# Optimization experiments

Measured on AMD Instinct MI355X. Metric: run time of the kernel, lower is better.

The kernel has to match this reference:

```python
import jax, jax.numpy as jnp
import numpy as np

B, S, D, C, I = 2, 1024, 1024, 64, 2048
N = S // C            # num_chunks (S divisible by C -> no padding)
EPS = 1e-6
BASE_LR = 0.01


def setup_inputs() -> dict:
    key = jax.random.key(0)
    ks = jax.random.split(key, 12)
    def xavier(k, shape):
        fan_in = shape[-1]
        return jax.random.normal(k, shape, jnp.float32) * (1.0 / np.sqrt(fan_in))
    return {
        "x": jax.random.normal(ks[0], (B, S, D), jnp.float32),
        "w1": xavier(ks[1], (I, D)),          # memory layer 0 weight [out,in]
        "w2": xavier(ks[2], (D, I)),          # memory layer 1 weight
        "ln_w": jnp.ones((D,), jnp.float32),  # memory RMSNorm weight
        "wq": xavier(ks[3], (D, D)),
        "wk": xavier(ks[4], (D, D)),
        "wv": xavier(ks[5], (D, D)),
        "qn_w": jnp.ones((D,), jnp.float32),
        "kn_w": jnp.ones((D,), jnp.float32),
        "alpha_w": jax.random.normal(ks[6], (1, C * D), jnp.float32) * 1e-3,
        "theta_w": jax.random.normal(ks[7], (1, C * D), jnp.float32) * 1e-3,
        "eta_w": jax.random.normal(ks[8], (1, C * D), jnp.float32) * 1e-3,
    }


def _rms(x, w):
    return x * jax.lax.rsqrt(jnp.mean(x * x, axis=-1, keepdims=True) + EPS) * w


def _memory_fwd(params, x):
    # 2-layer MLP memory with RMSNorm + residual
    w1, w2, lnw = params
    h = jax.nn.silu(x @ w1.T)
    y = h @ w2.T
    return x + _rms(y, lnw)


def _comb(e1, e2):
    # binary_operator: (a_j*a_i, kv_j + a_j*kv_i)
    a_i, kv_i = e1
    a_j, kv_j = e2
    return (a_j * a_i, kv_j + a_j * kv_i)


def _assocscan_update(pm, ps, g, eta, alpha):
    # pm,ps: [B,*s], g: [B,N,*s], eta/alpha: [B,N]
    extra = g.ndim - 2
    e = eta.reshape(eta.shape + (1,) * extra)
    a = alpha.reshape(alpha.shape + (1,) * extra)
    ones = jnp.ones_like(e[:, :1])
    # surprise recurrence: S_t = eta_t * S_{t-1} - g_t
    cS = jnp.concatenate([ones, e], axis=1)
    vS = jnp.concatenate([ps[:, None], -g], axis=1)
    _, Ssec = jax.lax.associative_scan(_comb, (cS, vS), axis=1)
    # memory recurrence: M_t = (1-alpha_t) * M_{t-1} + S_t
    cM = jnp.concatenate([ones, 1.0 - a], axis=1)
    vM = jnp.concatenate([pm[:, None], Ssec[:, 1:]], axis=1)
    _, Msec = jax.lax.associative_scan(_comb, (cM, vM), axis=1)
    return Msec[:, -1], Ssec[:, -1]


def reference(x, w1, w2, ln_w, wq, wk, wv, qn_w, kn_w, alpha_w, theta_w, eta_w):
    x4 = x.reshape(B, N, C, D)
    xc = x4.reshape(B, N, C * D)
    alpha = jax.nn.sigmoid(xc @ alpha_w.T)[..., 0]           # [B,N]
    theta = jax.nn.sigmoid(xc @ theta_w.T) * BASE_LR         # [B,N,1]
    eta = jax.nn.sigmoid(xc @ eta_w.T)[..., 0]               # [B,N]

    k = _rms(jax.nn.silu(x4 @ wk.T), kn_w)                   # [B,N,C,D]
    v = jax.nn.silu(x4 @ wv.T)                               # [B,N,C,D]

    # batched memory params (get_memory_params expands over batch)
    bw1 = jnp.broadcast_to(w1, (B,) + w1.shape)
    bw2 = jnp.broadcast_to(w2, (B,) + w2.shape)
    bln = jnp.broadcast_to(ln_w, (B,) + ln_w.shape)
    # initial surprises = 0
    s1 = jnp.zeros_like(bw1)
    s2 = jnp.zeros_like(bw2)
    sl = jnp.zeros_like(bln)

    def loss(p, ki, vi, th):
        pred = _memory_fwd(p, ki)
        return jnp.sum(jnp.mean((vi - pred) ** 2 * th, axis=-1))

    per_sample_grad = jax.vmap(jax.vmap(jax.grad(loss), in_axes=(None, 0, 0, 0)),
                               in_axes=(0, 0, 0, 0))
    g1, g2, gl = per_sample_grad((bw1, bw2, bln), k, v, theta)  # [B,N,*param]

    nw1, ns1 = _assocscan_update(bw1, s1, g1, eta, alpha)
    nw2, ns2 = _assocscan_update(bw2, s2, g2, eta, alpha)
    nln, nsl = _assocscan_update(bln, sl, gl, eta, alpha)

    # retrieve with updated memory
    q = _rms(jax.nn.silu(x4 @ wq.T), qn_w)                   # [B,N,C,D]
    out = jax.vmap(_memory_fwd)((nw1, nw2, nln), q)          # [B,N,C,D]
    out = out.reshape(B, S, D)
    return (out, nw1, nw2, nln, ns1, ns2, nsl)
```

## Files before the change

### kernel.cpp

```cpp
#include <hip/hip_runtime.h>

#define KD 1024
#define KI 2048
#define KB 2
#define KS 1024
#define KC 64
#define KN 16
#define KEPS 1e-6f

typedef __bf16 bf16x8 __attribute__((ext_vector_type(8)));
typedef __bf16 bf16x4 __attribute__((ext_vector_type(4)));
typedef float f32x4 __attribute__((ext_vector_type(4)));

__device__ __forceinline__ float sigf(float x){ return 1.0f/(1.0f+__expf(-x)); }
__device__ __forceinline__ float siluf(float x){ return x*sigf(x); }
__device__ __forceinline__ float dsiluf(float x){ float s=sigf(x); return s*(1.0f+x*(1.0f-s)); }

__device__ __forceinline__ void gld16(const __bf16* g, __bf16* l) {
  __builtin_amdgcn_global_load_lds(
    (const __attribute__((address_space(1))) unsigned int*)g,
    (__attribute__((address_space(3))) unsigned int*)l, 16, 0, 0);
}

#define WAIT_VM8()  asm volatile("s_waitcnt vmcnt(8)" ::: "memory")
#define WAIT_VM6()  asm volatile("s_waitcnt vmcnt(6)" ::: "memory")
#define WAIT_VM0()  asm volatile("s_waitcnt vmcnt(0)" ::: "memory")
#define WAIT_LGKM() asm volatile("s_waitcnt lgkmcnt(0)" ::: "memory")
#define BAR()       __builtin_amdgcn_s_barrier()

__device__ __forceinline__ void tconv_bodyP(float* T, const __bf16* in, __bf16* out,
                                            int R, int Cc, int bx, int by)
{
  const int r0 = by*64, c0 = bx*64;
  const int tx = threadIdx.x & 15, ty = threadIdx.x >> 4;
  #pragma unroll
  for (int i=0;i<4;i++){
    const int r = r0 + ty + i*16;
    const bf16x4 v = *(const bf16x4*)(in + (size_t)r*Cc + c0 + tx*4);
    T[(ty+i*16)*65 + tx*4+0]=(float)v[0]; T[(ty+i*16)*65 + tx*4+1]=(float)v[1];
    T[(ty+i*16)*65 + tx*4+2]=(float)v[2]; T[(ty+i*16)*65 + tx*4+3]=(float)v[3];
  }
  __syncthreads();
  #pragma unroll
  for (int i=0;i<4;i++){
    bf16x4 o = { (__bf16)T[(tx*4+0)*65 + ty+i*16], (__bf16)T[(tx*4+1)*65 + ty+i*16],
                 (__bf16)T[(tx*4+2)*65 + ty+i*16], (__bf16)T[(tx*4+3)*65 + ty+i*16] };
    *(bf16x4*)(out + (size_t)(c0+ty+i*16)*R + r0 + tx*4) = o;
  }
}

__device__ __forceinline__ void tconv_bodyF(const float* in, __bf16* out,
                                            int R, int Cc, int bx, int by)
{
  __shared__ float T[64][65];
  const int r0 = by*64, c0 = bx*64;
  const int tx = threadIdx.x & 15, ty = threadIdx.x >> 4;
  #pragma unroll
  for (int i=0;i<4;i++){
    const int r = r0 + ty + i*16;
    const float4 v = *(const float4*)(in + (size_t)r*Cc + c0 + tx*4);
    T[ty+i*16][tx*4+0]=v.x; T[ty+i*16][tx*4+1]=v.y;
    T[ty+i*16][tx*4+2]=v.z; T[ty+i*16][tx*4+3]=v.w;
  }
  __syncthreads();
  #pragma unroll
  for (int i=0;i<4;i++){
    bf16x4 o = { (__bf16)T[tx*4+0][ty+i*16], (__bf16)T[tx*4+1][ty+i*16],
                 (__bf16)T[tx*4+2][ty+i*16], (__bf16)T[tx*4+3][ty+i*16] };
    *(bf16x4*)(out + (size_t)(c0+ty+i*16)*R + r0 + tx*4) = o;
  }
}

__global__ __launch_bounds__(256) void prep_kernel(
  const float* __restrict__ x, const float* __restrict__ wk, const float* __restrict__ wv,
  const float* __restrict__ wq, const float* __restrict__ w1, const float* __restrict__ w2,
  const float* __restrict__ aw, const float* __restrict__ tw, const float* __restrict__ ew,
  __bf16* __restrict__ xb, __bf16* __restrict__ wkb, __bf16* __restrict__ wvb,
  __bf16* __restrict__ wqb, __bf16* __restrict__ w1b, __bf16* __restrict__ w2b,
  __bf16* __restrict__ w2tb, float* __restrict__ part, float* __restrict__ gl)
{
  const int g = blockIdx.x;
  if (g < 2048) {
    const int i = g*256 + threadIdx.x;
    const float4 xv = *(const float4*)(x + (size_t)i*4);
    bf16x4 o = { (__bf16)xv.x, (__bf16)xv.y, (__bf16)xv.z, (__bf16)xv.w };
    *(bf16x4*)(xb + (size_t)i*4) = o;
    const size_t co = (size_t)(i & 16383) * 4;
    const float4 av = *(const float4*)(aw + co);
    const float4 tv = *(const float4*)(tw + co);
    const float4 ev = *(const float4*)(ew + co);
    float da = xv.x*av.x + xv.y*av.y + xv.z*av.z + xv.w*av.w;
    float dt = xv.x*tv.x + xv.y*tv.y + xv.z*tv.z + xv.w*tv.w;
    float de = xv.x*ev.x + xv.y*ev.y + xv.z*ev.z + xv.w*ev.w;
    __shared__ float sA[256], sT[256], sE[256];
    sA[threadIdx.x]=da; sT[threadIdx.x]=dt; sE[threadIdx.x]=de;
    __syncthreads();
    for (int s=128;s>0;s>>=1){
      if ((int)threadIdx.x < s){
        sA[threadIdx.x]+=sA[threadIdx.x+s];
        sT[threadIdx.x]+=sT[threadIdx.x+s];
        sE[threadIdx.x]+=sE[threadIdx.x+s];
      }
      __syncthreads();
    }
    if (threadIdx.x==0){
      part[g] = sA[0]; part[2048+g] = sT[0]; part[4096+g] = sE[0];
    }
  } else if (g < 9216) {
    const long t = (long)g*256 + threadIdx.x;
    const float* s; __bf16* d; long i;
    if (t < 786432)       { s=wk; d=wkb; i=t-524288; }
    else if (t < 1048576) { s=wv; d=wvb; i=t-786432; }
    else if (t < 1310720) { s=wq; d=wqb; i=t-1048576; }
    else if (t < 1835008) { s=w1; d=w1b; i=t-1310720; }
    else                  { s=w2; d=w2b; i=t-1835008; }
    const float4 v = *(const float4*)(s + i*4);
    bf16x4 o = { (__bf16)v.x, (__bf16)v.y, (__bf16)v.z, (__bf16)v.w };
    *(bf16x4*)(d + i*4) = o;
  } else if (g < 9728) {
    const int gg = g - 9216;
    tconv_bodyF(w2, w2tb, 1024, 2048, gg & 31, gg >> 5);
  } else {
    const int gg = g - 9728;
    float4 z = {0.f,0.f,0.f,0.f};
    *(float4*)(gl + (size_t)gg*1024 + threadIdx.x*4) = z;
  }
}

template<int EPI, int MODE, int WT>
__device__ __forceinline__ void mgemm_body(
    __bf16* As, __bf16* Bs,
    const __bf16* __restrict__ A, const __bf16* __restrict__ B0,
    const __bf16* __restrict__ B1, const __bf16* __restrict__ B2,
    float* __restrict__ F0, float* __restrict__ F1,
    __bf16* __restrict__ Oa, __bf16* __restrict__ Ob, const __bf16* __restrict__ Aux,
    __bf16* __restrict__ OT, int ldt,
    int M, int Nn, int lda, int ldb, long bstr,
    int bx, int by, int bz)
{
  const int n0 = bx * 128;
  const int m0 = by * 128;
  const __bf16* Bp = B0;
  if (MODE==1) { if (bz==1) Bp=B1; else if (bz==2) Bp=B2; }
  float* F0p = F0;
  int koff0 = 0;
  if (MODE==2) koff0 = bz << 10;
  Bp += (size_t)(m0 >> 10) * (size_t)bstr;
  const int tid = threadIdx.x, wv = tid >> 6, lane = tid & 63;
  const int wm = (wv >> 1) << 6, wn = (wv & 1) << 6;
  const int fr = lane & 15, fg = lane >> 4;
  const int lr = lane >> 3, lc = lane & 7;
  const __bf16* asrc[4]; __bf16* adst[4];
  const __bf16* bsrc[4]; __bf16* bdst[4];
  #pragma unroll
  for (int i=0;i<4;i++){
    const int rowbase=(wv*4+i)*8, row=rowbase+lr;
    asrc[i] = A + (size_t)(m0+row)*lda + koff0 + ((lc^(row&7))<<3);
    adst[i] = As + rowbase*64;
    bsrc[i] = Bp + (size_t)(n0+row)*ldb + koff0 + ((lc^(row&7))<<3);
    bdst[i] = Bs + rowbase*64;
  }
  f32x4 acc[4][4] = {};
  #pragma unroll
  for (int i=0;i<4;i++) gld16(asrc[i], adst[i]);
  #pragma unroll
  for (int i=0;i<4;i++) gld16(bsrc[i], bdst[i]);
  WAIT_VM0();
  BAR();
  #pragma unroll 2
  for (int t=0;t<16;++t){
    const int p = t & 1;
    if (t < 15){
      const int ko = (t+1) << 6;
      const int q = p ^ 1;
      #pragma unroll
      for (int i=0;i<4;i++) gld16(asrc[i]+ko, adst[i]+q*8192);
      #pragma unroll
      for (int i=0;i<4;i++) gld16(bsrc[i]+ko, bdst[i]+q*8192);
      WAIT_VM8();
    } else {
      WAIT_VM0();
    }
    BAR();
    #pragma unroll
    for (int ks=0;ks<2;++ks){
      bf16x8 af[4], bfv[4];
      #pragma unroll
      for (int mi=0;mi<4;++mi){
        const int r = wm + mi*16 + fr;
        af[mi] = *(const bf16x8*)(As + p*8192 + r*64 + ((((ks<<2)+fg)^(r&7))<<3));
      }
      #pragma unroll
      for (int ni=0;ni<4;++ni){
        const int r = wn + ni*16 + fr;
        bfv[ni] = *(const bf16x8*)(Bs + p*8192 + r*64 + ((((ks<<2)+fg)^(r&7))<<3));
      }
      #pragma unroll
      for (int mi=0;mi<4;++mi)
        #pragma unroll
        for (int ni=0;ni<4;++ni)
          acc[mi][ni] = __builtin_amdgcn_mfma_f32_16x16x32_bf16(af[mi], bfv[ni], acc[mi][ni], 0,0,0);
    }
    WAIT_LGKM();
    BAR();
  }
  __bf16* T = As;
  #pragma unroll
  for (int mi=0;mi<4;++mi){
    #pragma unroll
    for (int ni=0;ni<4;++ni){
      bf16x4 tv;
      #pragma unroll
      for (int j=0;j<4;++j){
        const int m = m0 + wm + mi*16 + fg*4 + j;
        const int n = n0 + wn + ni*16 + fr;
        const size_t idx = (size_t)m * Nn + n;
        const float v = acc[mi][ni][j];
        float tval = 0.f;
        if (EPI==0) F0p[idx] = v;
        else if (EPI==2) { const float sv = siluf(v); Oa[idx]=(__bf16)sv; Ob[idx]=(__bf16)dsiluf(v); tval=sv; }
        else if (EPI==3) tval = v * (float)Aux[idx];
        else if (EPI==4) Oa[idx] = (__bf16)siluf(v);
        else if (EPI==5) {
          if (bz==0) F0[idx] = siluf(v);
          else if (bz==1) Oa[idx] = (__bf16)siluf(v);
          else F1[idx] = siluf(v);
        }
        else if (EPI==6) Oa[(size_t)bz*M*Nn + idx] = (__bf16)v;
        if (WT) tv[j] = (__bf16)tval;
      }
      if (WT){
        const int nl = wn + ni*16 + fr;
        const int ml = wm + mi*16 + fg*4;
        *(bf16x4*)(T + nl*128 + (ml ^ ((nl&7)<<3))) = tv;
      }
    }
  }
  if (WT){
    __syncthreads();
    const int tn = tid >> 1, tc = tid & 1;
    #pragma unroll
    for (int u=0;u<8;++u){
      const int m8 = (tc*8+u)*8;
      const bf16x8 v = *(const bf16x8*)(T + tn*128 + (m8 ^ ((tn&7)<<3)));
      *(bf16x8*)(OT + (size_t)(n0+tn)*ldt + m0 + m8) = v;
    }
  }
}

template<int EPI, int MODE, int WT>
__global__ __launch_bounds__(256) void mgemm3(
    const __bf16* __restrict__ A, const __bf16* __restrict__ B0,
    const __bf16* __restrict__ B1, const __bf16* __restrict__ B2,
    float* __restrict__ F0, float* __restrict__ F1,
    __bf16* __restrict__ Oa, __bf16* __restrict__ Ob, const __bf16* __restrict__ Aux,
    __bf16* __restrict__ OT, int ldt,
    int M, int Nn, int lda, int ldb, long bstr)
{
  __shared__ __bf16 As[2*128*64];
  __shared__ __bf16 Bs[2*128*64];
  mgemm_body<EPI,MODE,WT>(As, Bs, A, B0, B1, B2, F0, F1, Oa, Ob, Aux, OT, ldt,
                          M, Nn, lda, ldb, bstr, blockIdx.x, blockIdx.y, blockIdx.z);
}

__global__ __launch_bounds__(256) void gemm_a_kernel(
    const __bf16* __restrict__ kb16, const __bf16* __restrict__ w1b,
    __bf16* __restrict__ hb16, __bf16* __restrict__ db16, __bf16* __restrict__ hT,
    __bf16* __restrict__ kT)
{
  __shared__ __bf16 As[2*128*64];
  __shared__ __bf16 Bs[2*128*64];
  const int g = blockIdx.x;
  if (g < 256)
    mgemm_body<2,0,1>(As, Bs, kb16, w1b, nullptr, nullptr, nullptr, nullptr,
                      hb16, db16, nullptr, hT, 2048, 2048, 2048, 1024, 1024, 0,
                      g & 15, g >> 4, 0);
  else {
    const int t = g - 256;
    tconv_bodyP((float*)As, kb16, kT, 2048, 1024, t & 15, t >> 4);
  }
}

__global__ __launch_bounds__(256) void gemm_ga_kernel(
    const __bf16* __restrict__ gyb, const __bf16* __restrict__ w2tb,
    const __bf16* __restrict__ db16, __bf16* __restrict__ gaT,
    __bf16* __restrict__ gyT)
{
  __shared__ __bf16 As[2*128*64];
  __shared__ __bf16 Bs[2*128*64];
  const int g = blockIdx.x;
  if (g < 256)
    mgemm_body<3,0,1>(As, Bs, gyb, w2tb, nullptr, nullptr, nullptr, nullptr,
                      nullptr, nullptr, db16, gaT, 2048, 2048, 2048, 1024, 1024, 0,
                      g & 15, g >> 4, 0);
  else {
    const int t = g - 256;
    tconv_bodyP((float*)As, gyb, gyT, 2048, 1024, t & 15, t >> 4);
  }
}

__device__ __forceinline__ void wacc_body(
    __bf16* As, __bf16* Bs,
    const __bf16* __restrict__ A, const __bf16* __restrict__ B,
    const float* __restrict__ Winit,
    const float* __restrict__ cm, const float* __restrict__ cs,
    const float* __restrict__ Pw,
    float* __restrict__ outM, __bf16* __restrict__ outMb, float* __restrict__ outS,
    int M, int Nn, int lda, int ldb, int n0, int m0, int bz)
{
  const int koff0 = bz << 10;
  const int tid = threadIdx.x, wv = tid >> 6, lane = tid & 63;
  const int wm = (wv >> 1) << 6, wn = (wv & 1) << 5;
  const int fr = lane & 15, fg = lane >> 4;
  const int lr = lane >> 3, lc = lane & 7;
  float cmr[KN], csr[KN];
  #pragma unroll
  for (int n=0;n<KN;n++){ cmr[n]=cm[bz*KN+n]; csr[n]=cs[bz*KN+n]; }
  const __bf16* asrc[4]; __bf16* adst[4];
  const __bf16* bsrc[2]; __bf16* bdst[2];
  #pragma unroll
  for (int i=0;i<4;i++){
    const int rowbase=(wv*4+i)*8, row=rowbase+lr;
    asrc[i] = A + (size_t)(m0+row)*lda + koff0 + ((lc^(row&7))<<3);
    adst[i] = As + rowbase*64;
  }
  #pragma unroll
  for (int i=0;i<2;i++){
    const int rowbase=(wv*2+i)*8, row=rowbase+lr;
    bsrc[i] = B + (size_t)(n0+row)*ldb + koff0 + ((lc^(row&7))<<3);
    bdst[i] = Bs + rowbase*64;
  }
  f32x4 accM[4][2] = {}, accS[4][2] = {};
  asm volatile("s_waitcnt vmcnt(0) lgkmcnt(0)" ::: "memory");
  #pragma unroll
  for (int i=0;i<4;i++) gld16(asrc[i], adst[i]);
  #pragma unroll
  for (int i=0;i<2;i++) gld16(bsrc[i], bdst[i]);
  WAIT_VM0();
  BAR();
  #pragma unroll 2
  for (int t=0;t<16;++t){
    const int p = t & 1;
    const float cmc = cmr[t], csc = csr[t];
    if (t < 15){
      const int ko = (t+1) << 6;
      const int q = p ^ 1;
      #pragma unroll
      for (int i=0;i<4;i++) gld16(asrc[i]+ko, adst[i]+q*8192);
      #pragma unroll
      for (int i=0;i<2;i++) gld16(bsrc[i]+ko, bdst[i]+q*4096);
      WAIT_VM6();
    } else {
      WAIT_VM0();
    }
    BAR();
    bf16x8 a0[4], a1[4], b0[2], b1[2];
    #pragma unroll
    for (int mi=0;mi<4;++mi){
      const int r = wm + mi*16 + fr;
      a0[mi] = *(const bf16x8*)(As + p*8192 + r*64 + (((0+fg)^(r&7))<<3));
      a1[mi] = *(const bf16x8*)(As + p*8192 + r*64 + (((4+fg)^(r&7))<<3));
    }
    #pragma unroll
    for (int ni=0;ni<2;++ni){
      const int r = wn + ni*16 + fr;
      b0[ni] = *(const bf16x8*)(Bs + p*4096 + r*64 + (((0+fg)^(r&7))<<3));
      b1[ni] = *(const bf16x8*)(Bs + p*4096 + r*64 + (((4+fg)^(r&7))<<3));
    }
    #pragma unroll
    for (int mi=0;mi<4;++mi){
      #pragma unroll
      for (int ni=0;ni<2;++ni){
        const f32x4 zf = {0.f,0.f,0.f,0.f};
        f32x4 P = __builtin_amdgcn_mfma_f32_16x16x32_bf16(a0[mi], b0[ni], zf, 0,0,0);
        P = __builtin_amdgcn_mfma_f32_16x16x32_bf16(a1[mi], b1[ni], P, 0,0,0);
        accM[mi][ni] += P * cmc;
        accS[mi][ni] += P * csc;
      }
    }
    WAIT_LGKM();
    BAR();
  }
  const float pw = Pw[bz];
  #pragma unroll
  for (int mi=0;mi<4;++mi){
    #pragma unroll
    for (int ni=0;ni<2;++ni){
      #pragma unroll
      for (int j=0;j<4;++j){
        const int m = m0 + wm + mi*16 + fg*4 + j;
        const int n = n0 + wn + ni*16 + fr;
        const size_t widx = (size_t)m * Nn + n;
        const size_t oidx = (size_t)bz * M * Nn + widx;
        const float vm = pw * Winit[widx] + accM[mi][ni][j];
        outM[oidx] = vm;
        outMb[oidx] = (__bf16)vm;
        outS[oidx] = accS[mi][ni][j];
      }
    }
  }
}

__global__ __launch_bounds__(256) void waccall_kernel(
    const __bf16* __restrict__ gaT, const __bf16* __restrict__ kT, const float* __restrict__ w1,
    const __bf16* __restrict__ gyT, const __bf16* __restrict__ hT, const float* __restrict__ w2,
    const float* __restrict__ gl, const float* __restrict__ lnw,
    const float* __restrict__ cm, const float* __restrict__ cs, const float* __restrict__ Pw,
    float* __restrict__ nw1, __bf16* __restrict__ nw1b, float* __restrict__ ns1,
    float* __restrict__ nw2, __bf16* __restrict__ nw2b, float* __restrict__ ns2,
    float* __restrict__ nln, float* __restrict__ nsl)
{
  __shared__ __bf16 As[2*128*64];
  __shared__ __bf16 Bs[2*64*64];
  const int g = blockIdx.x;
  if (g < 512){
    const int bz = g >> 8, rem = g & 255;
    wacc_body(As, Bs, gaT, kT, w1, cm, cs, Pw, nw1, nw1b, ns1,
              2048, 1024, 2048, 2048, (rem & 15)*64, (rem >> 4)*128, bz);
  } else if (g < 1024){
    const int t = g - 512;
    const int bz = t >> 8, rem = t & 255;
    wacc_body(As, Bs, gyT, hT, w2, cm, cs, Pw, nw2, nw2b, ns2,
              1024, 2048, 2048, 2048, (rem & 31)*64, (rem >> 5)*128, bz);
  } else {
    const int idx = (g - 1024)*256 + threadIdx.x;
    const int b = idx >> 10, d = idx & (KD-1);
    float am=0.f, as=0.f;
    for (int n=0;n<KN;n++){
      const float gv = gl[(size_t)(b*KN+n)*KD + d];
      am += cm[b*KN+n]*gv; as += cs[b*KN+n]*gv;
    }
    nln[idx] = Pw[b]*lnw[d] + am;
    nsl[idx] = as;
  }
}

__global__ __launch_bounds__(256) void rmsfuse_kernel(
    const float* __restrict__ kv, const float* __restrict__ kw, __bf16* __restrict__ k16,
    const float* __restrict__ qv, const float* __restrict__ qw, __bf16* __restrict__ q16,
    const float* __restrict__ part, float* __restrict__ cm, float* __restrict__ cs,
    float* __restrict__ Pw, float* __restrict__ theta)
{
  if (blockIdx.y == 2){
    if (blockIdx.x != 0) return;
    __shared__ float P[32][8][3];
    const int bn = threadIdx.x >> 3, sg = threadIdx.x & 7;
    float s0=0.f, s1=0.f, s2=0.f;
    #pragma unroll
    for (int u=0;u<8;u++){
      const int seg = bn*64 + sg*8 + u;
      s0 += part[seg]; s1 += part[2048+seg]; s2 += part[4096+seg];
    }
    P[bn][sg][0]=s0; P[bn][sg][1]=s1; P[bn][sg][2]=s2;
    __syncthreads();
    if ((int)threadIdx.x < KB){
      const int b = threadIdx.x;
      float al[KN], et[KN];
      for (int n=0;n<KN;n++){
        const int c = b*KN+n;
        float sa=0.f, st=0.f, se=0.f;
        #pragma unroll
        for (int k=0;k<8;k++){ sa+=P[c][k][0]; st+=P[c][k][1]; se+=P[c][k][2]; }
        al[n]=sigf(sa); theta[c]=sigf(st)*0.01f; et[n]=sigf(se);
      }
      float prodE = 1.f;
      for (int j=KN-1;j>=0;j--){ cs[b*KN+j] = -prodE; prodE *= et[j]; }
      float Ac[KN]; Ac[KN-1]=1.f;
      for (int t=KN-2;t>=0;t--) Ac[t] = Ac[t+1]*(1.f-al[t+1]);
      for (int j=0;j<KN;j++){
        float inner=0.f, E=1.f;
        for (int t=j;t<KN;t++){ inner += Ac[t]*E; if (t+1<KN) E *= et[t+1]; }
        cm[b*KN+j] = -inner;
      }
      float pw=1.f;
      for (int n=0;n<KN;n++) pw *= (1.f-al[n]);
      Pw[b]=pw;
    }
    return;
  }
  const float* v; const float* w; __bf16* o16;
  if (blockIdx.y == 0){ v=kv; w=kw; o16=k16; } else { v=qv; w=qw; o16=q16; }
  const int row = blockIdx.x * 4 + (threadIdx.x >> 6);
  const int lane = threadIdx.x & 63;
  const float* p = v + (size_t)row * KD;
  __bf16* p16 = o16 + (size_t)row * KD;
  float vals[16]; float ss = 0.f;
  #pragma unroll
  for (int l=0;l<16;l++){ vals[l] = p[lane + (l<<6)]; ss += vals[l]*vals[l]; }
  #pragma unroll
  for (int o=32;o>0;o>>=1) ss += __shfl_xor(ss, o, 64);
  const float inv = rsqrtf(ss * (1.0f/KD) + KEPS);
  #pragma unroll
  for (int l=0;l<16;l++){
    const int d = lane + (l<<6);
    p16[d] = (__bf16)(vals[l]*inv*w[d]);
  }
}

__global__ __launch_bounds__(256) void rms_grad_kernel(
    const __bf16* __restrict__ y16,
    const __bf16* __restrict__ k16, const __bf16* __restrict__ v16,
    const float* __restrict__ lnw, const float* __restrict__ theta,
    __bf16* __restrict__ gy, float* __restrict__ gl)
{
  const int wv = threadIdx.x >> 6;
  const int row = blockIdx.x * 4 + wv;
  const int lane = threadIdx.x & 63;
  const int chunk = blockIdx.x >> 4;
  const float th2 = theta[chunk] * (2.0f / KD);
  const __bf16* yr0 = y16 + (size_t)row * KD;
  const __bf16* yr1 = y16 + 2097152 + (size_t)row * KD;
  const __bf16* kr = k16 + (size_t)row * KD;
  const __bf16* vr = v16 + (size_t)row * KD;
  float yv[16]; float ss = 0.f;
  #pragma unroll
  for (int l=0;l<16;l++){
    const int d = lane + (l<<6);
    yv[l] = (float)yr0[d] + (float)yr1[d]; ss += yv[l]*yv[l];
  }
  #pragma unroll
  for (int o=32;o>0;o>>=1) ss += __shfl_xor(ss, o, 64);
  const float inv = rsqrtf(ss * (1.0f/KD) + KEPS);
  float gzv[16]; float sdot = 0.f;
  #pragma unroll
  for (int l=0;l<16;l++){
    const int d = lane + (l<<6);
    const float gz = th2 * ((float)kr[d] + yv[l]*inv*lnw[d] - (float)vr[d]);
    gzv[l] = gz;
    sdot += gz * lnw[d] * yv[l];
  }
  #pragma unroll
  for (int o=32;o>0;o>>=1) sdot += __shfl_xor(sdot, o, 64);
  const float c3 = inv*inv*inv * (1.0f/KD) * sdot;
  __bf16* gyr = gy + (size_t)row * KD;
  __shared__ float L[4][KD];
  #pragma unroll
  for (int l=0;l<16;l++){
    const int d = lane + (l<<6);
    gyr[d] = (__bf16)(inv * lnw[d] * gzv[l] - c3 * yv[l]);
    L[wv][d] = gzv[l] * yv[l] * inv;
  }
  __syncthreads();
  if (wv == 0){
    float* glc = gl + (size_t)chunk * KD;
    #pragma unroll
    for (int l=0;l<16;l++){
      const int d = lane + (l<<6);
      atomicAdd(&glc[d], L[0][d]+L[1][d]+L[2][d]+L[3][d]);
    }
  }
}

__global__ __launch_bounds__(256) void final_out_kernel(
    const __bf16* __restrict__ q16, const __bf16* __restrict__ yq16,
    const float* __restrict__ nln, float* __restrict__ out)
{
  const int row = blockIdx.x * 4 + (threadIdx.x >> 6);
  const int lane = threadIdx.x & 63;
  const int b = row >> 10;
  float yv[16]; float ss = 0.f;
  #pragma unroll
  for (int l=0;l<16;l++){
    const int d = lane + (l<<6);
    yv[l] = (float)yq16[(size_t)row*KD + d] + (float)yq16[2097152 + (size_t)row*KD + d];
    ss += yv[l]*yv[l];
  }
  #pragma unroll
  for (int o=32;o>0;o>>=1) ss += __shfl_xor(ss, o, 64);
  const float inv = rsqrtf(ss * (1.0f/KD) + KEPS);
  #pragma unroll
  for (int l=0;l<16;l++){
    const int d = lane + (l<<6);
    out[(size_t)row*KD + d] = (float)q16[(size_t)row*KD + d] + yv[l]*inv*nln[b*KD + d];
  }
}

extern "C" void kernel_launch(void* const* d_in, const int* in_sizes, int n_in,
                              void* d_out, int out_size, void* d_ws, size_t ws_size,
                              hipStream_t stream)
{
  const float* x    = (const float*)d_in[0];
  const float* w1   = (const float*)d_in[1];
  const float* w2   = (const float*)d_in[2];
  const float* lnw  = (const float*)d_in[3];
  const float* wq   = (const float*)d_in[4];
  const float* wk   = (const float*)d_in[5];
  const float* wv   = (const float*)d_in[6];
  const float* qnw  = (const float*)d_in[7];
  const float* knw  = (const float*)d_in[8];
  const float* aw   = (const float*)d_in[9];
  const float* tw   = (const float*)d_in[10];
  const float* ew   = (const float*)d_in[11];

  float* out = (float*)d_out;
  float* nw1 = out + (size_t)KB*KS*KD;
  float* nw2 = nw1 + (size_t)KB*KI*KD;
  float* nln = nw2 + (size_t)KB*KD*KI;
  float* ns1 = nln + (size_t)KB*KD;
  float* ns2 = ns1 + (size_t)KB*KI*KD;
  float* nsl = ns2 + (size_t)KB*KD*KI;

  float* ws = (float*)d_ws;
  size_t o = 0;
  float* kbuf = ws+o; o += 2097152;
  float* qbuf = ws+o; o += 2097152;
  float* gl   = ws+o; o += 32768;
  float* part = ws+o; o += 6144;
  float* cmb  = ws+o; o += 32;
  float* csb  = ws+o; o += 32;
  float* Pwb  = ws+o; o += 32;
  float* thetab = ws+o; o += 32;
  __bf16* bb = (__bf16*)(ws + o);
  size_t p = 0;
  __bf16* xb   = bb+p; p += 2097152;
  __bf16* wkb  = bb+p; p += 1048576;
  __bf16* wvb  = bb+p; p += 1048576;
  __bf16* wqb  = bb+p; p += 1048576;
  __bf16* w1b  = bb+p; p += 2097152;
  __bf16* w2b  = bb+p; p += 2097152;
  __bf16* w2tb = bb+p; p += 2097152;
  __bf16* kb16 = bb+p; p += 2097152;
  __bf16* qb16 = bb+p; p += 2097152;
  __bf16* vb16 = bb+p; p += 2097152;
  __bf16* hb16 = bb+p; p += 4194304;
  __bf16* db16 = bb+p; p += 4194304;
  __bf16* hT   = bb+p; p += 4194304;
  __bf16* gaT  = bb+p; p += 4194304;
  __bf16* nw1b = bb+p; p += 4194304;
  __bf16* nw2b = bb+p; p += 4194304;
  __bf16* y16  = bb+p; p += 4194304;
  __bf16* gyT = xb;
  __bf16* kT  = wkb;
  __bf16* gyb = w1b;
  __bf16* hq16= w2b;

  dim3 blk(256);

  prep_kernel<<<9760, blk, 0, stream>>>(x, wk, wv, wq, w1, w2, aw, tw, ew,
      xb, wkb, wvb, wqb, w1b, w2b, w2tb, part, gl);
  mgemm3<5,1,0><<<dim3(8,16,3), blk, 0, stream>>>(xb, wkb, wvb, wqb,
      kbuf, qbuf, vb16, nullptr, nullptr, nullptr, 0, 2048, 1024, 1024, 1024, 0);
  rmsfuse_kernel<<<dim3(512,3), blk, 0, stream>>>(kbuf, knw, kb16, qbuf, qnw, qb16,
      part, cmb, csb, Pwb, thetab);
  gemm_a_kernel<<<768, blk, 0, stream>>>(kb16, w1b, hb16, db16, hT, kT);
  mgemm3<6,2,0><<<dim3(8,16,2), blk, 0, stream>>>(hb16, w2b, nullptr, nullptr,
      nullptr, nullptr, y16, nullptr, nullptr, nullptr, 0, 2048, 1024, 2048, 2048, 0);
  rms_grad_kernel<<<512, blk, 0, stream>>>(y16, kb16, vb16, lnw, thetab, gyb, gl);
  gemm_ga_kernel<<<768, blk, 0, stream>>>(gyb, w2tb, db16, gaT, gyT);
  waccall_kernel<<<1032, blk, 0, stream>>>(gaT, kT, w1, gyT, hT, w2, gl, lnw,
      cmb, csb, Pwb, nw1, nw1b, ns1, nw2, nw2b, ns2, nln, nsl);
  mgemm3<4,0,0><<<dim3(16,16,1), blk, 0, stream>>>(qb16, nw1b, nullptr, nullptr,
      nullptr, nullptr, hq16, nullptr, nullptr, nullptr, 0, 2048, 2048, 1024, 1024, (long)KI*KD);
  mgemm3<6,2,0><<<dim3(8,16,2), blk, 0, stream>>>(hq16, nw2b, nullptr, nullptr,
      nullptr, nullptr, y16, nullptr, nullptr, nullptr, 0, 2048, 1024, 2048, 2048, (long)KD*KI);
  final_out_kernel<<<512, blk, 0, stream>>>(qb16, y16, nln, out);
}
```

Baseline: 231.6 us.

## Shrink GEMM tiles to 128x64 and read bf16 initial weights in update

The shared GEMM body moves from 128x128 to 128x64 output tiles. That halves the B-operand shared-memory buffer and the accumulator array, and all GEMM launches use twice as many blocks, so the 256 CUs get more blocks and better wave quantization. The weight-update kernel now reads the bf16 copies of w1/w2 as the initial memory weights instead of the fp32 originals, which cuts its read traffic but rounds the initial weights into nw1/nw2. Scratch buffer aliasing is reshuffled so w1b/w2b stay valid until that kernel runs. The trade-off is lower data reuse per tile and a small accuracy loss in the returned weights.

New measurement: 195.8 us. 1.18x faster.

```diff
diff --git a/kernel.cpp b/kernel.cpp
--- a/kernel.cpp
+++ b/kernel.cpp
@@ -22,7 +22,6 @@
     (__attribute__((address_space(3))) unsigned int*)l, 16, 0, 0);
 }
 
-#define WAIT_VM8()  asm volatile("s_waitcnt vmcnt(8)" ::: "memory")
 #define WAIT_VM6()  asm volatile("s_waitcnt vmcnt(6)" ::: "memory")
 #define WAIT_VM0()  asm volatile("s_waitcnt vmcnt(0)" ::: "memory")
 #define WAIT_LGKM() asm volatile("s_waitcnt lgkmcnt(0)" ::: "memory")
@@ -138,33 +137,37 @@
     int M, int Nn, int lda, int ldb, long bstr,
     int bx, int by, int bz)
 {
-  const int n0 = bx * 128;
+  const int n0 = bx * 64;
   const int m0 = by * 128;
   const __bf16* Bp = B0;
   if (MODE==1) { if (bz==1) Bp=B1; else if (bz==2) Bp=B2; }
   float* F0p = F0;
   int koff0 = 0;
-  if (MODE==2) koff0 = bz << 10;
+  if (MODE==2) { koff0 = bz << 10; }
   Bp += (size_t)(m0 >> 10) * (size_t)bstr;
   const int tid = threadIdx.x, wv = tid >> 6, lane = tid & 63;
-  const int wm = (wv >> 1) << 6, wn = (wv & 1) << 6;
+  const int wm = (wv >> 1) << 6, wn = (wv & 1) << 5;
   const int fr = lane & 15, fg = lane >> 4;
   const int lr = lane >> 3, lc = lane & 7;
   const __bf16* asrc[4]; __bf16* adst[4];
-  const __bf16* bsrc[4]; __bf16* bdst[4];
+  const __bf16* bsrc[2]; __bf16* bdst[2];
   #pragma unroll
   for (int i=0;i<4;i++){
     const int rowbase=(wv*4+i)*8, row=rowbase+lr;
     asrc[i] = A + (size_t)(m0+row)*lda + koff0 + ((lc^(row&7))<<3);
     adst[i] = As + rowbase*64;
+  }
+  #pragma unroll
+  for (int i=0;i<2;i++){
+    const int rowbase=(wv*2+i)*8, row=rowbase+lr;
     bsrc[i] = Bp + (size_t)(n0+row)*ldb + koff0 + ((lc^(row&7))<<3);
     bdst[i] = Bs + rowbase*64;
   }
-  f32x4 acc[4][4] = {};
+  f32x4 acc[4][2] = {};
   #pragma unroll
   for (int i=0;i<4;i++) gld16(asrc[i], adst[i]);
   #pragma unroll
-  for (int i=0;i<4;i++) gld16(bsrc[i], bdst[i]);
+  for (int i=0;i<2;i++) gld16(bsrc[i], bdst[i]);
   WAIT_VM0();
   BAR();
   #pragma unroll 2
@@ -176,29 +179,29 @@
       #pragma unroll
       for (int i=0;i<4;i++) gld16(asrc[i]+ko, adst[i]+q*8192);
       #pragma unroll
-      for (int i=0;i<4;i++) gld16(bsrc[i]+ko, bdst[i]+q*8192);
-      WAIT_VM8();
+      for (int i=0;i<2;i++) gld16(bsrc[i]+ko, bdst[i]+q*4096);
+      WAIT_VM6();
     } else {
       WAIT_VM0();
     }
     BAR();
     #pragma unroll
     for (int ks=0;ks<2;++ks){
-      bf16x8 af[4], bfv[4];
+      bf16x8 af[4], bfv[2];
       #pragma unroll
       for (int mi=0;mi<4;++mi){
         const int r = wm + mi*16 + fr;
         af[mi] = *(const bf16x8*)(As + p*8192 + r*64 + ((((ks<<2)+fg)^(r&7))<<3));
       }
       #pragma unroll
-      for (int ni=0;ni<4;++ni){
+      for (int ni=0;ni<2;++ni){
         const int r = wn + ni*16 + fr;
-        bfv[ni] = *(const bf16x8*)(Bs + p*8192 + r*64 + ((((ks<<2)+fg)^(r&7))<<3));
+        bfv[ni] = *(const bf16x8*)(Bs + p*4096 + r*64 + ((((ks<<2)+fg)^(r&7))<<3));
       }
       #pragma unroll
       for (int mi=0;mi<4;++mi)
         #pragma unroll
-        for (int ni=0;ni<4;++ni)
+        for (int ni=0;ni<2;++ni)
           acc[mi][ni] = __builtin_amdgcn_mfma_f32_16x16x32_bf16(af[mi], bfv[ni], acc[mi][ni], 0,0,0);
     }
     WAIT_LGKM();
@@ -208,7 +211,7 @@
   #pragma unroll
   for (int mi=0;mi<4;++mi){
     #pragma unroll
-    for (int ni=0;ni<4;++ni){
+    for (int ni=0;ni<2;++ni){
       bf16x4 tv;
       #pragma unroll
       for (int j=0;j<4;++j){
@@ -238,10 +241,10 @@
   }
   if (WT){
     __syncthreads();
-    const int tn = tid >> 1, tc = tid & 1;
-    #pragma unroll
-    for (int u=0;u<8;++u){
-      const int m8 = (tc*8+u)*8;
+    const int tn = tid >> 2, tc = tid & 3;
+    #pragma unroll
+    for (int u=0;u<4;++u){
+      const int m8 = tc*32 + u*8;
       const bf16x8 v = *(const bf16x8*)(T + tn*128 + (m8 ^ ((tn&7)<<3)));
       *(bf16x8*)(OT + (size_t)(n0+tn)*ldt + m0 + m8) = v;
     }
@@ -249,7 +252,7 @@
 }
 
 template<int EPI, int MODE, int WT>
-__global__ __launch_bounds__(256) void mgemm3(
+__global__ __launch_bounds__(256) void mgemm2(
     const __bf16* __restrict__ A, const __bf16* __restrict__ B0,
     const __bf16* __restrict__ B1, const __bf16* __restrict__ B2,
     float* __restrict__ F0, float* __restrict__ F1,
@@ -258,7 +261,7 @@
     int M, int Nn, int lda, int ldb, long bstr)
 {
   __shared__ __bf16 As[2*128*64];
-  __shared__ __bf16 Bs[2*128*64];
+  __shared__ __bf16 Bs[2*64*64];
   mgemm_body<EPI,MODE,WT>(As, Bs, A, B0, B1, B2, F0, F1, Oa, Ob, Aux, OT, ldt,
                           M, Nn, lda, ldb, bstr, blockIdx.x, blockIdx.y, blockIdx.z);
 }
@@ -269,14 +272,14 @@
     __bf16* __restrict__ kT)
 {
   __shared__ __bf16 As[2*128*64];
-  __shared__ __bf16 Bs[2*128*64];
+  __shared__ __bf16 Bs[2*64*64];
   const int g = blockIdx.x;
-  if (g < 256)
+  if (g < 512)
     mgemm_body<2,0,1>(As, Bs, kb16, w1b, nullptr, nullptr, nullptr, nullptr,
                       hb16, db16, nullptr, hT, 2048, 2048, 2048, 1024, 1024, 0,
-                      g & 15, g >> 4, 0);
+                      g & 31, g >> 5, 0);
   else {
-    const int t = g - 256;
+    const int t = g - 512;
     tconv_bodyP((float*)As, kb16, kT, 2048, 1024, t & 15, t >> 4);
   }
 }
@@ -287,14 +290,14 @@
     __bf16* __restrict__ gyT)
 {
   __shared__ __bf16 As[2*128*64];
-  __shared__ __bf16 Bs[2*128*64];
+  __shared__ __bf16 Bs[2*64*64];
   const int g = blockIdx.x;
-  if (g < 256)
+  if (g < 512)
     mgemm_body<3,0,1>(As, Bs, gyb, w2tb, nullptr, nullptr, nullptr, nullptr,
                       nullptr, nullptr, db16, gaT, 2048, 2048, 2048, 1024, 1024, 0,
-                      g & 15, g >> 4, 0);
+                      g & 31, g >> 5, 0);
   else {
-    const int t = g - 256;
+    const int t = g - 512;
     tconv_bodyP((float*)As, gyb, gyT, 2048, 1024, t & 15, t >> 4);
   }
 }
@@ -302,7 +305,7 @@
 __device__ __forceinline__ void wacc_body(
     __bf16* As, __bf16* Bs,
     const __bf16* __restrict__ A, const __bf16* __restrict__ B,
-    const float* __restrict__ Winit,
+    const __bf16* __restrict__ Winit,
     const float* __restrict__ cm, const float* __restrict__ cs,
     const float* __restrict__ Pw,
     float* __restrict__ outM, __bf16* __restrict__ outMb, float* __restrict__ outS,
@@ -392,7 +395,7 @@
         const int n = n0 + wn + ni*16 + fr;
         const size_t widx = (size_t)m * Nn + n;
         const size_t oidx = (size_t)bz * M * Nn + widx;
-        const float vm = pw * Winit[widx] + accM[mi][ni][j];
+        const float vm = pw * (float)Winit[widx] + accM[mi][ni][j];
         outM[oidx] = vm;
         outMb[oidx] = (__bf16)vm;
         outS[oidx] = accS[mi][ni][j];
@@ -402,8 +405,8 @@
 }
 
 __global__ __launch_bounds__(256) void waccall_kernel(
-    const __bf16* __restrict__ gaT, const __bf16* __restrict__ kT, const float* __restrict__ w1,
-    const __bf16* __restrict__ gyT, const __bf16* __restrict__ hT, const float* __restrict__ w2,
+    const __bf16* __restrict__ gaT, const __bf16* __restrict__ kT, const __bf16* __restrict__ w1b,
+    const __bf16* __restrict__ gyT, const __bf16* __restrict__ hT, const __bf16* __restrict__ w2b,
     const float* __restrict__ gl, const float* __restrict__ lnw,
     const float* __restrict__ cm, const float* __restrict__ cs, const float* __restrict__ Pw,
     float* __restrict__ nw1, __bf16* __restrict__ nw1b, float* __restrict__ ns1,
@@ -415,12 +418,12 @@
   const int g = blockIdx.x;
   if (g < 512){
     const int bz = g >> 8, rem = g & 255;
-    wacc_body(As, Bs, gaT, kT, w1, cm, cs, Pw, nw1, nw1b, ns1,
+    wacc_body(As, Bs, gaT, kT, w1b, cm, cs, Pw, nw1, nw1b, ns1,
               2048, 1024, 2048, 2048, (rem & 15)*64, (rem >> 4)*128, bz);
   } else if (g < 1024){
     const int t = g - 512;
     const int bz = t >> 8, rem = t & 255;
-    wacc_body(As, Bs, gyT, hT, w2, cm, cs, Pw, nw2, nw2b, ns2,
+    wacc_body(As, Bs, gyT, hT, w2b, cm, cs, Pw, nw2, nw2b, ns2,
               1024, 2048, 2048, 2048, (rem & 31)*64, (rem >> 5)*128, bz);
   } else {
     const int idx = (g - 1024)*256 + threadIdx.x;
@@ -631,27 +634,27 @@
   __bf16* y16  = bb+p; p += 4194304;
   __bf16* gyT = xb;
   __bf16* kT  = wkb;
-  __bf16* gyb = w1b;
-  __bf16* hq16= w2b;
+  __bf16* gyb = (__bf16*)kbuf;
+  __bf16* hq16= (__bf16*)qbuf;
 
   dim3 blk(256);
 
   prep_kernel<<<9760, blk, 0, stream>>>(x, wk, wv, wq, w1, w2, aw, tw, ew,
       xb, wkb, wvb, wqb, w1b, w2b, w2tb, part, gl);
-  mgemm3<5,1,0><<<dim3(8,16,3), blk, 0, stream>>>(xb, wkb, wvb, wqb,
+  mgemm2<5,1,0><<<dim3(16,16,3), blk, 0, stream>>>(xb, wkb, wvb, wqb,
       kbuf, qbuf, vb16, nullptr, nullptr, nullptr, 0, 2048, 1024, 1024, 1024, 0);
   rmsfuse_kernel<<<dim3(512,3), blk, 0, stream>>>(kbuf, knw, kb16, qbuf, qnw, qb16,
       part, cmb, csb, Pwb, thetab);
-  gemm_a_kernel<<<768, blk, 0, stream>>>(kb16, w1b, hb16, db16, hT, kT);
-  mgemm3<6,2,0><<<dim3(8,16,2), blk, 0, stream>>>(hb16, w2b, nullptr, nullptr,
+  gemm_a_kernel<<<1024, blk, 0, stream>>>(kb16, w1b, hb16, db16, hT, kT);
+  mgemm2<6,2,0><<<dim3(16,16,2), blk, 0, stream>>>(hb16, w2b, nullptr, nullptr,
       nullptr, nullptr, y16, nullptr, nullptr, nullptr, 0, 2048, 1024, 2048, 2048, 0);
   rms_grad_kernel<<<512, blk, 0, stream>>>(y16, kb16, vb16, lnw, thetab, gyb, gl);
-  gemm_ga_kernel<<<768, blk, 0, stream>>>(gyb, w2tb, db16, gaT, gyT);
-  waccall_kernel<<<1032, blk, 0, stream>>>(gaT, kT, w1, gyT, hT, w2, gl, lnw,
+  gemm_ga_kernel<<<1024, blk, 0, stream>>>(gyb, w2tb, db16, gaT, gyT);
+  waccall_kernel<<<1032, blk, 0, stream>>>(gaT, kT, w1b, gyT, hT, w2b, gl, lnw,
       cmb, csb, Pwb, nw1, nw1b, ns1, nw2, nw2b, ns2, nln, nsl);
-  mgemm3<4,0,0><<<dim3(16,16,1), blk, 0, stream>>>(qb16, nw1b, nullptr, nullptr,
+  mgemm2<4,0,0><<<dim3(32,16,1), blk, 0, stream>>>(qb16, nw1b, nullptr, nullptr,
       nullptr, nullptr, hq16, nullptr, nullptr, nullptr, 0, 2048, 2048, 1024, 1024, (long)KI*KD);
-  mgemm3<6,2,0><<<dim3(8,16,2), blk, 0, stream>>>(hq16, nw2b, nullptr, nullptr,
+  mgemm2<6,2,0><<<dim3(16,16,2), blk, 0, stream>>>(hq16, nw2b, nullptr, nullptr,
       nullptr, nullptr, y16, nullptr, nullptr, nullptr, 0, 2048, 1024, 2048, 2048, (long)KD*KI);
   final_out_kernel<<<512, blk, 0, stream>>>(qb16, y16, nln, out);
 }
```
